# Kernel tuning notes

Hardware: AMD Instinct MI355X
Metric: run time of the kernel (lower is better)

The kernel has to match this reference:

```python
import math
import jax, jax.numpy as jnp
import numpy as np

VOCAB = 80; MAX_SEQ_LEN = 32; D_MODEL = 512; NHEAD = 8; DFF = 2048; NLAYERS = 6
EOS = 1; SOS = 2; PAD = 0; BATCH = 8; MEM_LEN = 256; PE_LEN = MAX_SEQ_LEN + 2
EPS = 1e-5


def _sinusoid(max_len, d):
    pos = np.arange(max_len)[:, None].astype(np.float32)
    div = np.exp(np.arange(0, d, 2).astype(np.float32) * -(math.log(10000.0) / d))
    pe = np.zeros((max_len, d), np.float32)
    pe[:, 0::2] = np.sin(pos * div)
    pe[:, 1::2] = np.cos(pos * div)
    return jnp.asarray(pe)


def setup_inputs() -> dict:
    key = jax.random.key(0)
    ks = jax.random.split(key, 10)
    s = 0.02
    def n(k, shape, scale=s):
        return jax.random.normal(k, shape, jnp.float32) * scale
    return {
        "memory": n(ks[0], (BATCH, MEM_LEN, D_MODEL), 1.0),
        "emb_table": n(ks[1], (VOCAB, D_MODEL), 1.0),
        "pe": _sinusoid(PE_LEN, D_MODEL),
        "sa_in_w": n(ks[2], (NLAYERS, 3 * D_MODEL, D_MODEL)),
        "sa_in_b": jnp.zeros((NLAYERS, 3 * D_MODEL), jnp.float32),
        "sa_out_w": n(ks[3], (NLAYERS, D_MODEL, D_MODEL)),
        "sa_out_b": jnp.zeros((NLAYERS, D_MODEL), jnp.float32),
        "ca_in_w": n(ks[4], (NLAYERS, 3 * D_MODEL, D_MODEL)),
        "ca_in_b": jnp.zeros((NLAYERS, 3 * D_MODEL), jnp.float32),
        "ca_out_w": n(ks[5], (NLAYERS, D_MODEL, D_MODEL)),
        "ca_out_b": jnp.zeros((NLAYERS, D_MODEL), jnp.float32),
        "ln_w": jnp.ones((NLAYERS, 3, D_MODEL), jnp.float32),
        "ln_b": jnp.zeros((NLAYERS, 3, D_MODEL), jnp.float32),
        "ff1_w": n(ks[6], (NLAYERS, DFF, D_MODEL)),
        "ff1_b": jnp.zeros((NLAYERS, DFF), jnp.float32),
        "ff2_w": n(ks[7], (NLAYERS, D_MODEL, DFF)),
        "ff2_b": jnp.zeros((NLAYERS, D_MODEL), jnp.float32),
        "clf_w": n(ks[8], (VOCAB, D_MODEL)),
        "clf_b": jnp.zeros((VOCAB,), jnp.float32),
    }


def _layer_norm(x, g, b):
    mu = jnp.mean(x, -1, keepdims=True)
    var = jnp.mean((x - mu) ** 2, -1, keepdims=True)
    return (x - mu) * jax.lax.rsqrt(var + EPS) * g + b


def _mha(q_in, kv_in, in_w, in_b, out_w, out_b, mask):
    d = q_in.shape[-1]; hd = d // NHEAD
    wq, wk, wv = jnp.split(in_w, 3, 0)
    bq, bk, bv = jnp.split(in_b, 3)
    B, Tq, _ = q_in.shape; Tk = kv_in.shape[1]
    q = (q_in @ wq.T + bq).reshape(B, Tq, NHEAD, hd)
    k = (kv_in @ wk.T + bk).reshape(B, Tk, NHEAD, hd)
    v = (kv_in @ wv.T + bv).reshape(B, Tk, NHEAD, hd)
    scores = jnp.einsum('bqhd,bkhd->bhqk', q, k) / math.sqrt(hd)
    if mask is not None:
        scores = jnp.where(mask, -1e9, scores)
    probs = jax.nn.softmax(scores, -1)
    out = jnp.einsum('bhqk,bkhd->bqhd', probs, v).reshape(B, Tq, d)
    return out @ out_w.T + out_b


def _decoder(tgt, memory, causal, p):
    # post-norm TransformerDecoder (torch default, dropout=identity at inference)
    x = tgt
    for l in range(NLAYERS):
        x = _layer_norm(x + _mha(x, x, p['sa_in_w'][l], p['sa_in_b'][l], p['sa_out_w'][l], p['sa_out_b'][l], causal), p['ln_w'][l, 0], p['ln_b'][l, 0])
        x = _layer_norm(x + _mha(x, memory, p['ca_in_w'][l], p['ca_in_b'][l], p['ca_out_w'][l], p['ca_out_b'][l], None), p['ln_w'][l, 1], p['ln_b'][l, 1])
        h = jax.nn.gelu(x @ p['ff1_w'][l].T + p['ff1_b'][l], approximate=False)
        x = _layer_norm(x + h @ p['ff2_w'][l].T + p['ff2_b'][l], p['ln_w'][l, 2], p['ln_b'][l, 2])
    return x


def _greedy(memory, emb_table, pe, p, clf_w, clf_b):
    B = memory.shape[0]; T1 = MAX_SEQ_LEN + 1
    sq = math.sqrt(D_MODEL)
    causal = jnp.triu(jnp.ones((T1, T1), bool), 1)[None, None]  # True = blocked
    tgt0 = jnp.zeros((B, T1, D_MODEL), memory.dtype)
    tgt0 = tgt0.at[:, 0].set(pe[0] + emb_table[SOS] * sq)

    def step(tgt, t):
        # full recompute of the whole decoder stack each step (no KV cache),
        # causal mask makes position t depend only on the valid prefix.
        out = _decoder(tgt, memory, causal, p)
        out_t = jax.lax.dynamic_slice_in_dim(out, t, 1, 1)[:, 0]
        logits = out_t @ clf_w.T + clf_b
        pred = jnp.argmax(logits, -1)
        # original uses pe[len(sampled_ids)] == pe[t+2] for the token at slot t+1
        new_e = jnp.take(pe, t + 2, axis=0) + emb_table[pred] * sq
        tgt = jax.lax.dynamic_update_slice_in_dim(tgt, new_e[:, None, :], t + 1, 1)
        return tgt, (logits, pred)

    _, (logits, preds) = jax.lax.scan(step, tgt0, jnp.arange(MAX_SEQ_LEN))
    all_logits = jnp.transpose(logits, (1, 0, 2))  # [B, T, V]
    sampled = jnp.concatenate([jnp.full((B, 1), SOS, preds.dtype), preds.T], 1)
    eos_idx = jnp.argmax(sampled == EOS, 1)  # first eos (0 if none, as torch)
    sampled = jnp.where(jnp.arange(T1)[None] <= eos_idx[:, None], PAD, sampled)
    return all_logits, sampled


def reference(memory, emb_table, pe, sa_in_w, sa_in_b, sa_out_w, sa_out_b, ca_in_w, ca_in_b, ca_out_w, ca_out_b, ln_w, ln_b, ff1_w, ff1_b, ff2_w, ff2_b, clf_w, clf_b):
    p = dict(sa_in_w=sa_in_w, sa_in_b=sa_in_b, sa_out_w=sa_out_w, sa_out_b=sa_out_b,
             ca_in_w=ca_in_w, ca_in_b=ca_in_b, ca_out_w=ca_out_w, ca_out_b=ca_out_b,
             ln_w=ln_w, ln_b=ln_b, ff1_w=ff1_w, ff1_b=ff1_b, ff2_w=ff2_w, ff2_b=ff2_b)
    return _greedy(memory, emb_table, pe, p, clf_w, clf_b)
```

## Files before the change

kernel.cpp:

```cpp
#include <hip/hip_runtime.h>
#include <math.h>

constexpr int T1 = 33, NL = 6, VOC = 80;
constexpr float SQD = 22.62741699796952f;

__device__ float g_memk[(size_t)NL * 2048 * 512];
__device__ float g_memv[(size_t)NL * 2048 * 512];
__device__ float g_kc[(size_t)NL * 8 * T1 * 512];
__device__ float g_vc[(size_t)NL * 8 * T1 * 512];
__device__ float g_x[8 * 512], g_x2[8 * 512], g_y[8 * 512], g_q[8 * 512], g_att[8 * 512];
__device__ float g_h[8 * 2048];
__device__ int   g_tok[8 * T1];

struct DecP {
  const float *mem, *emb, *pe, *saw, *sab, *sow, *sob, *caw, *cab, *cow, *cob,
              *lnw, *lnb, *f1w, *f1b, *f2w, *f2b, *cw, *cb;
  float* out;
};

__global__ __launch_bounds__(256) void k_memkv(const float* __restrict__ mem,
                                               const float* __restrict__ caw,
                                               const float* __restrict__ cab) {
  __shared__ float mlds[128][34];
  __shared__ float wlds[256][34];
  const int tid = threadIdx.x;
  const int l = blockIdx.x / 64, rem = blockIdx.x % 64;
  const int mt = rem >> 2, rt = rem & 3;
  const float* wbase = caw + (size_t)l * 1536 * 512 + (size_t)512 * 512;

  float acc[8][16];
#pragma unroll
  for (int i = 0; i < 8; ++i)
#pragma unroll
    for (int j = 0; j < 16; ++j) acc[i][j] = 0.f;

  const int tm = tid >> 4, tr = tid & 15;

  for (int kb = 0; kb < 16; ++kb) {
    __syncthreads();
    {
      int row = tid >> 1, half = tid & 1;
      const float2* src = (const float2*)(mem + (size_t)(mt * 128 + row) * 512 + kb * 32 + half * 16);
      float2* dst = (float2*)&mlds[row][half * 16];
#pragma unroll
      for (int q = 0; q < 8; ++q) dst[q] = src[q];
    }
    {
      int c2 = (tid & 15) * 2, rb = tid >> 4;
#pragma unroll
      for (int q = 0; q < 16; ++q) {
        int row = rb + 16 * q;
        *(float2*)&wlds[row][c2] =
            *(const float2*)(wbase + (size_t)(rt * 256 + row) * 512 + kb * 32 + c2);
      }
    }
    __syncthreads();
#pragma unroll 4
    for (int k2 = 0; k2 < 16; ++k2) {
      float2 mv[8];
#pragma unroll
      for (int i = 0; i < 8; ++i) mv[i] = *(const float2*)&mlds[tm * 8 + i][2 * k2];
#pragma unroll
      for (int j = 0; j < 16; ++j) {
        float2 w2 = *(const float2*)&wlds[tr + 16 * j][2 * k2];
#pragma unroll
        for (int i = 0; i < 8; ++i) acc[i][j] += mv[i].x * w2.x + mv[i].y * w2.y;
      }
    }
  }
#pragma unroll
  for (int i = 0; i < 8; ++i) {
    int mrow = mt * 128 + tm * 8 + i;
#pragma unroll
    for (int j = 0; j < 16; ++j) {
      int r = rt * 256 + tr + 16 * j;
      float v = acc[i][j] + cab[l * 1536 + 512 + r];
      if (r < 512) g_memk[((size_t)l * 2048 + mrow) * 512 + r] = v;
      else         g_memv[((size_t)l * 2048 + mrow) * 512 + (r - 512)] = v;
    }
  }
}

__device__ __forceinline__ float wave_reduce8(const float (&acc)[8], int lane) {
  float a0, a1, a2, a3;
  {
    bool hi = lane & 1;
    float s0 = hi ? acc[0] : acc[1], s1 = hi ? acc[2] : acc[3];
    float s2 = hi ? acc[4] : acc[5], s3 = hi ? acc[6] : acc[7];
    float r0 = __shfl_xor(s0, 1), r1 = __shfl_xor(s1, 1);
    float r2 = __shfl_xor(s2, 1), r3 = __shfl_xor(s3, 1);
    a0 = (hi ? acc[1] : acc[0]) + r0;  a1 = (hi ? acc[3] : acc[2]) + r1;
    a2 = (hi ? acc[5] : acc[4]) + r2;  a3 = (hi ? acc[7] : acc[6]) + r3;
  }
  float b0, b1;
  {
    bool hi = lane & 2;
    float s0 = hi ? a0 : a1, s1 = hi ? a2 : a3;
    float r0 = __shfl_xor(s0, 2), r1 = __shfl_xor(s1, 2);
    b0 = (hi ? a1 : a0) + r0;  b1 = (hi ? a3 : a2) + r1;
  }
  float f;
  {
    bool hi = lane & 4;
    float s = hi ? b0 : b1;
    float r = __shfl_xor(s, 4);
    f = (hi ? b1 : b0) + r;
  }
  f += __shfl_xor(f, 8);  f += __shfl_xor(f, 16);  f += __shfl_xor(f, 32);
  return f;
}

__device__ __forceinline__ void stage_in(float (*sx)[520], const float* __restrict__ g,
                                         bool doLN, const float* __restrict__ lw,
                                         const float* __restrict__ lb, float* __restrict__ wb) {
  const int tid = threadIdx.x;
#pragma unroll
  for (int q = 0; q < 4; ++q) {
    int f4 = tid + 256 * q;
    int b = f4 >> 7, c = (f4 & 127) << 2;
    float4 v = ((const float4*)g)[f4];
    *(float4*)&sx[b][c] = v;
  }
  __syncthreads();
  if (doLN) {
    const int lane = tid & 63, wv = tid >> 6;
#pragma unroll
    for (int rr = 0; rr < 2; ++rr) {
      int b = wv + 4 * rr;
      float vals[8]; float sm = 0.f;
#pragma unroll
      for (int j = 0; j < 8; ++j) { vals[j] = sx[b][lane + 64 * j]; sm += vals[j]; }
#pragma unroll
      for (int o = 32; o; o >>= 1) sm += __shfl_xor(sm, o);
      float mu = sm * (1.f / 512.f);
      float s2 = 0.f;
#pragma unroll
      for (int j = 0; j < 8; ++j) { float d = vals[j] - mu; s2 += d * d; }
#pragma unroll
      for (int o = 32; o; o >>= 1) s2 += __shfl_xor(s2, o);
      float rstd = 1.f / sqrtf(s2 * (1.f / 512.f) + 1e-5f);
#pragma unroll
      for (int j = 0; j < 8; ++j) {
        int c = lane + 64 * j;
        sx[b][c] = (vals[j] - mu) * rstd * lw[c] + lb[c];
      }
    }
    __syncthreads();
  }
  if (wb && blockIdx.x == 0) {
#pragma unroll
    for (int q = 0; q < 4; ++q) {
      int f4 = tid + 256 * q;
      int b = f4 >> 7, c = (f4 & 127) << 2;
      ((float4*)wb)[f4] = *(float4*)&sx[b][c];
    }
  }
}

template <int MODE>
__device__ __forceinline__ void gemv512(float (*sx)[520], const float* __restrict__ W,
                                        const float* __restrict__ bias, int rpb,
                                        float* __restrict__ out, const float* __restrict__ res,
                                        int l, int t) {
  const int lane = threadIdx.x & 63, wv = threadIdx.x >> 6;
  const int r0 = blockIdx.x * rpb;
  for (int rr = wv; rr < rpb; rr += 4) {
    const int r = r0 + rr;
    const float* wr = W + (size_t)r * 512;
    float acc[8] = {0, 0, 0, 0, 0, 0, 0, 0};
#pragma unroll
    for (int j = 0; j < 8; ++j) {
      float w = wr[lane + 64 * j];
#pragma unroll
      for (int b = 0; b < 8; ++b) acc[b] += w * sx[b][lane + 64 * j];
    }
    float f = wave_reduce8(acc, lane);
    if (lane < 8) {
      const int b = lane;
      float v = f + bias[r];
      if constexpr (MODE == 0) {
        if (r < 512)       out[b * 512 + r] = v;
        else if (r < 1024) g_kc[(((size_t)l * 8 + b) * T1 + t) * 512 + (r - 512)] = v;
        else               g_vc[(((size_t)l * 8 + b) * T1 + t) * 512 + (r - 1024)] = v;
      } else if constexpr (MODE == 1) {
        out[b * 512 + r] = v + res[b * 512 + r];
      } else if constexpr (MODE == 2) {
        out[b * 512 + r] = v;
      } else {
        out[b * 2048 + r] = 0.5f * v * (1.f + erff(v * 0.70710678118654752f));
      }
    }
  }
}

__device__ __forceinline__ void stage_h(float (*sb)[2052]) {
  const int tid = threadIdx.x;
#pragma unroll
  for (int q = 0; q < 16; ++q) {
    int f4 = tid + 256 * q;
    int b = f4 >> 9, c = (f4 & 511) << 2;
    *(float4*)&sb[b][c] = ((const float4*)g_h)[f4];
  }
}

__device__ __forceinline__ void gemvH(float (*sb)[2052], const float* __restrict__ W,
                                      const float* __restrict__ bias,
                                      const float* __restrict__ res, float* __restrict__ out) {
  const int lane = threadIdx.x & 63, wv = threadIdx.x >> 6;
  const int r0 = blockIdx.x * 8;
  for (int rr = wv; rr < 8; rr += 4) {
    const int r = r0 + rr;
    const float* wr = W + (size_t)r * 2048;
    float acc[8] = {0, 0, 0, 0, 0, 0, 0, 0};
#pragma unroll 8
    for (int j = 0; j < 32; ++j) {
      float w = wr[lane + 64 * j];
#pragma unroll
      for (int b = 0; b < 8; ++b) acc[b] += w * sb[b][lane + 64 * j];
    }
    float f = wave_reduce8(acc, lane);
    if (lane < 8) out[lane * 512 + r] = f + bias[r] + res[lane * 512 + r];
  }
}

__global__ __launch_bounds__(256) void k_start(DecP P) {
  int b = blockIdx.x;
#pragma unroll
  for (int q = 0; q < 2; ++q) {
    int c = threadIdx.x + 256 * q;
    g_x[b * 512 + c] = P.pe[c] + P.emb[2 * 512 + c] * SQD;
  }
  if (threadIdx.x == 0) g_tok[b * T1] = 2;
}

__global__ __launch_bounds__(256) void k_A(DecP P, int l, int t) {
  __shared__ float sx[8][520];
  const float* lw = (l > 0) ? P.lnw + ((l - 1) * 3 + 2) * 512 : P.lnw;
  const float* lb = (l > 0) ? P.lnb + ((l - 1) * 3 + 2) * 512 : P.lnb;
  stage_in(sx, (l == 0) ? g_x : g_y, l > 0, lw, lb, (l > 0) ? g_x : nullptr);
  gemv512<0>(sx, P.saw + (size_t)l * 1536 * 512, P.sab + l * 1536, 8, g_q, nullptr, l, t);
}

__global__ __launch_bounds__(64) void k_B(DecP P, int l, int t) {
  __shared__ float s_p[128];
  const int lane = threadIdx.x;
  const int b = blockIdx.x >> 3, h = blockIdx.x & 7;
  s_p[lane] = g_q[b * 512 + h * 64 + lane];
  asm volatile("s_waitcnt lgkmcnt(0)" ::: "memory");
  __builtin_amdgcn_sched_barrier(0);
  float sc = -3.4e38f;
  if (lane <= t) {
    const float4* kr = (const float4*)&g_kc[(((size_t)l * 8 + b) * T1 + lane) * 512 + h * 64];
    float s = 0.f;
#pragma unroll
    for (int d4 = 0; d4 < 16; ++d4) {
      float4 kv = kr[d4];
      s += s_p[d4 * 4 + 0] * kv.x + s_p[d4 * 4 + 1] * kv.y +
           s_p[d4 * 4 + 2] * kv.z + s_p[d4 * 4 + 3] * kv.w;
    }
    sc = s * 0.125f;
  }
  float m = sc;
#pragma unroll
  for (int o = 32; o; o >>= 1) m = fmaxf(m, __shfl_xor(m, o));
  float ex = (lane <= t) ? expf(sc - m) : 0.f;
  float sum = ex;
#pragma unroll
  for (int o = 32; o; o >>= 1) sum += __shfl_xor(sum, o);
  s_p[64 + lane] = ex / sum;
  asm volatile("s_waitcnt lgkmcnt(0)" ::: "memory");
  __builtin_amdgcn_sched_barrier(0);
  float o = 0.f;
  for (int j = 0; j <= t; ++j)
    o += s_p[64 + j] * g_vc[(((size_t)l * 8 + b) * T1 + j) * 512 + h * 64 + lane];
  g_att[b * 512 + h * 64 + lane] = o;
}

__global__ __launch_bounds__(256) void k_C(DecP P, int l) {
  __shared__ float sx[8][520];
  stage_in(sx, g_att, false, nullptr, nullptr, nullptr);
  gemv512<1>(sx, P.sow + (size_t)l * 512 * 512, P.sob + l * 512, 8, g_y, g_x, l, 0);
}

__global__ __launch_bounds__(256) void k_D(DecP P, int l) {
  __shared__ float sx[8][520];
  stage_in(sx, g_y, true, P.lnw + (l * 3 + 0) * 512, P.lnb + (l * 3 + 0) * 512, g_x2);
  gemv512<2>(sx, P.caw + (size_t)l * 1536 * 512, P.cab + l * 1536, 8, g_q, nullptr, l, 0);
}

__global__ __launch_bounds__(256) void k_E(DecP P, int l) {
  __shared__ float s_p[336];
  __shared__ float s_w[4][2];
  __shared__ float s_pv[4][64];
  const int tid = threadIdx.x;
  const int lane = tid & 63, wv = tid >> 6;
  const int b = blockIdx.x >> 3, h = blockIdx.x & 7;
  if (tid < 64) s_p[tid] = g_q[b * 512 + h * 64 + tid];
  __syncthreads();
  int m0 = wv * 64 + lane;
  const float4* kr = (const float4*)&g_memk[((size_t)l * 2048 + b * 256 + m0) * 512 + h * 64];
  float s = 0.f;
#pragma unroll
  for (int d4 = 0; d4 < 16; ++d4) {
    float4 kv = kr[d4];
    s += s_p[d4 * 4 + 0] * kv.x + s_p[d4 * 4 + 1] * kv.y +
         s_p[d4 * 4 + 2] * kv.z + s_p[d4 * 4 + 3] * kv.w;
  }
  s *= 0.125f;
  float m = s;
#pragma unroll
  for (int o = 32; o; o >>= 1) m = fmaxf(m, __shfl_xor(m, o));
  if (lane == 0) s_w[wv][0] = m;
  __syncthreads();
  float M = fmaxf(fmaxf(s_w[0][0], s_w[1][0]), fmaxf(s_w[2][0], s_w[3][0]));
  float ex = expf(s - M);
  float sum = ex;
#pragma unroll
  for (int o = 32; o; o >>= 1) sum += __shfl_xor(sum, o);
  if (lane == 0) s_w[wv][1] = sum;
  __syncthreads();
  float S = s_w[0][1] + s_w[1][1] + s_w[2][1] + s_w[3][1];
  s_p[64 + m0] = ex / S;
  __syncthreads();
  float o = 0.f;
  const float* vbase = &g_memv[((size_t)l * 2048 + b * 256) * 512 + h * 64];
  for (int j = 0; j < 64; ++j) {
    int mm = wv * 64 + j;
    o += s_p[64 + mm] * vbase[(size_t)mm * 512 + lane];
  }
  s_pv[wv][lane] = o;
  __syncthreads();
  if (wv == 0) {
    float tot = s_pv[0][lane] + s_pv[1][lane] + s_pv[2][lane] + s_pv[3][lane];
    g_att[b * 512 + h * 64 + lane] = tot;
  }
}

__global__ __launch_bounds__(256) void k_F(DecP P, int l) {
  __shared__ float sx[8][520];
  stage_in(sx, g_att, false, nullptr, nullptr, nullptr);
  gemv512<1>(sx, P.cow + (size_t)l * 512 * 512, P.cob + l * 512, 8, g_y, g_x2, l, 0);
}

__global__ __launch_bounds__(256) void k_G(DecP P, int l) {
  __shared__ float sx[8][520];
  stage_in(sx, g_y, true, P.lnw + (l * 3 + 1) * 512, P.lnb + (l * 3 + 1) * 512, g_x2);
  gemv512<3>(sx, P.f1w + (size_t)l * 2048 * 512, P.f1b + l * 2048, 8, g_h, nullptr, l, 0);
}

__global__ __launch_bounds__(256) void k_H(DecP P, int l) {
  __shared__ float sb[8][2052];
  stage_h(sb);
  __syncthreads();
  gemvH(sb, P.f2w + (size_t)l * 512 * 2048, P.f2b + l * 512, g_x2, g_y);
}

__global__ __launch_bounds__(256) void k_T(DecP P, int t) {
  __shared__ float sx[8][520];
  __shared__ float s_p[80];
  __shared__ int s_int[1];
  const int tid = threadIdx.x;
  const int lane = tid & 63, wv = tid >> 6;
  const int b = blockIdx.x;
  stage_in(sx, g_y, true, P.lnw + (5 * 3 + 2) * 512, P.lnb + (5 * 3 + 2) * 512, nullptr);
  for (int i = 0; i < 20; ++i) {
    int r = wv * 20 + i;
    const float* wr = P.cw + (size_t)r * 512;
    float a = 0.f;
#pragma unroll
    for (int j = 0; j < 8; ++j) a += wr[lane + 64 * j] * sx[b][lane + 64 * j];
#pragma unroll
    for (int o = 32; o; o >>= 1) a += __shfl_xor(a, o);
    if (lane == 0) {
      float v = a + P.cb[r];
      s_p[r] = v;
      P.out[((size_t)b * 32 + t) * VOC + r] = v;
    }
  }
  __syncthreads();
  if (wv == 0) {
    float v1 = s_p[lane];
    int i1 = lane;
    if (lane < 16) {
      float v2 = s_p[64 + lane];
      if (v2 > v1) { v1 = v2; i1 = 64 + lane; }
    }
#pragma unroll
    for (int o = 32; o; o >>= 1) {
      float ov = __shfl_xor(v1, o);
      int oi = __shfl_xor(i1, o);
      if (ov > v1 || (ov == v1 && oi < i1)) { v1 = ov; i1 = oi; }
    }
    if (lane == 0) { s_int[0] = i1; g_tok[b * T1 + t + 1] = i1; }
  }
  __syncthreads();
  int pred = s_int[0];
#pragma unroll
  for (int q = 0; q < 2; ++q) {
    int c = tid + 256 * q;
    g_x[b * 512 + c] = P.pe[(t + 2) * 512 + c] + P.emb[(size_t)pred * 512 + c] * SQD;
  }
}

__global__ __launch_bounds__(64) void k_out(DecP P) {
  int lane = threadIdx.x;
  if (lane < 8) {
    int b = lane;
    int eos = -1;
    for (int j = 0; j < T1; ++j) {
      int tk = g_tok[b * T1 + j];
      if (tk == 1 && eos < 0) eos = j;
    }
    if (eos < 0) eos = 0;
    for (int j = 0; j < T1; ++j) {
      int tk = g_tok[b * T1 + j];
      P.out[20480 + b * T1 + j] = (j <= eos) ? 0.f : (float)tk;
    }
  }
}

extern "C" void kernel_launch(void* const* d_in, const int* in_sizes, int n_in,
                              void* d_out, int out_size, void* d_ws, size_t ws_size,
                              hipStream_t stream) {
  (void)in_sizes; (void)n_in; (void)d_ws; (void)ws_size; (void)out_size;
  const float* mem = (const float*)d_in[0];
  const float* emb = (const float*)d_in[1];
  const float* pe  = (const float*)d_in[2];
  const float* saw = (const float*)d_in[3];
  const float* sab = (const float*)d_in[4];
  const float* sow = (const float*)d_in[5];
  const float* sob = (const float*)d_in[6];
  const float* caw = (const float*)d_in[7];
  const float* cab = (const float*)d_in[8];
  const float* cow = (const float*)d_in[9];
  const float* cob = (const float*)d_in[10];
  const float* lnw = (const float*)d_in[11];
  const float* lnb = (const float*)d_in[12];
  const float* f1w = (const float*)d_in[13];
  const float* f1b = (const float*)d_in[14];
  const float* f2w = (const float*)d_in[15];
  const float* f2b = (const float*)d_in[16];
  const float* cw  = (const float*)d_in[17];
  const float* cb  = (const float*)d_in[18];

  DecP P{mem, emb, pe, saw, sab, sow, sob, caw, cab, cow, cob,
         lnw, lnb, f1w, f1b, f2w, f2b, cw, cb, (float*)d_out};

  hipLaunchKernelGGL(k_start, dim3(8), dim3(256), 0, stream, P);
  hipLaunchKernelGGL(k_memkv, dim3(384), dim3(256), 0, stream, mem, caw, cab);

  for (int t = 0; t < 32; ++t) {
    for (int l = 0; l < NL; ++l) {
      hipLaunchKernelGGL(k_A, dim3(192), dim3(256), 0, stream, P, l, t);
      hipLaunchKernelGGL(k_B, dim3(64), dim3(64), 0, stream, P, l, t);
      hipLaunchKernelGGL(k_C, dim3(64), dim3(256), 0, stream, P, l);
      hipLaunchKernelGGL(k_D, dim3(64), dim3(256), 0, stream, P, l);
      hipLaunchKernelGGL(k_E, dim3(64), dim3(256), 0, stream, P, l);
      hipLaunchKernelGGL(k_F, dim3(64), dim3(256), 0, stream, P, l);
      hipLaunchKernelGGL(k_G, dim3(256), dim3(256), 0, stream, P, l);
      hipLaunchKernelGGL(k_H, dim3(64), dim3(256), 0, stream, P, l);
    }
    hipLaunchKernelGGL(k_T, dim3(8), dim3(256), 0, stream, P, t);
  }
  hipLaunchKernelGGL(k_out, dim3(1), dim3(64), 0, stream, P);
}
```

Measured before the change: 8.999 ms.

## Fuse decoder layer into three per-(batch,head) kernels with double-precision partial sums

Replaces the eight launches per layer with three fused kernels, each run by 64 blocks with one block per (batch, head). Each kernel does the projection, attention and output projection for its head and writes per-head partial sums. The next kernel reduces those partials and fuses bias, residual and LayerNorm. Memory K/V is relaid as [l][b][h][m][d] so each head's slice is contiguous. All accumulation moves to double precision, presumably so greedy argmax tokens match the reference, but FP64 math and the extra partial-sum traffic add cost that may offset the launch savings.

After: 34.63 ms. +284.9%, slower.

```diff
diff --git a/kernel.cpp b/kernel.cpp
--- a/kernel.cpp
+++ b/kernel.cpp
@@ -4,12 +4,16 @@
 constexpr int T1 = 33, NL = 6, VOC = 80;
 constexpr float SQD = 22.62741699796952f;
 
-__device__ float g_memk[(size_t)NL * 2048 * 512];
-__device__ float g_memv[(size_t)NL * 2048 * 512];
+__device__ float g_memk[(size_t)NL * 8 * 8 * 256 * 64];
+__device__ float g_memv[(size_t)NL * 8 * 8 * 256 * 64];
 __device__ float g_kc[(size_t)NL * 8 * T1 * 512];
 __device__ float g_vc[(size_t)NL * 8 * T1 * 512];
-__device__ float g_x[8 * 512], g_x2[8 * 512], g_y[8 * 512], g_q[8 * 512], g_att[8 * 512];
-__device__ float g_h[8 * 2048];
+__device__ float g_cur[8 * 512];
+__device__ float g_x2[8 * 512];
+__device__ float g_x3[8 * 512];
+__device__ double g_part1[8 * 512 * 8];
+__device__ double g_part2[8 * 512 * 8];
+__device__ double g_part3[8 * 512 * 8];
 __device__ int   g_tok[8 * T1];
 
 struct DecP {
@@ -71,156 +75,82 @@
 #pragma unroll
   for (int i = 0; i < 8; ++i) {
     int mrow = mt * 128 + tm * 8 + i;
+    int bb = mrow >> 8, mm = mrow & 255;
 #pragma unroll
     for (int j = 0; j < 16; ++j) {
       int r = rt * 256 + tr + 16 * j;
       float v = acc[i][j] + cab[l * 1536 + 512 + r];
-      if (r < 512) g_memk[((size_t)l * 2048 + mrow) * 512 + r] = v;
-      else         g_memv[((size_t)l * 2048 + mrow) * 512 + (r - 512)] = v;
-    }
-  }
-}
-
-__device__ __forceinline__ float wave_reduce8(const float (&acc)[8], int lane) {
-  float a0, a1, a2, a3;
+      if (r < 512) {
+        int hh = r >> 6, d = r & 63;
+        g_memk[((((size_t)l * 8 + bb) * 8 + hh) * 256 + mm) * 64 + d] = v;
+      } else {
+        int r2 = r - 512, hh = r2 >> 6, d = r2 & 63;
+        g_memv[((((size_t)l * 8 + bb) * 8 + hh) * 256 + mm) * 64 + d] = v;
+      }
+    }
+  }
+}
+
+__device__ __forceinline__ double wave_reduce8d(const double (&acc)[8], int lane) {
+  double a0, a1, a2, a3;
   {
     bool hi = lane & 1;
-    float s0 = hi ? acc[0] : acc[1], s1 = hi ? acc[2] : acc[3];
-    float s2 = hi ? acc[4] : acc[5], s3 = hi ? acc[6] : acc[7];
-    float r0 = __shfl_xor(s0, 1), r1 = __shfl_xor(s1, 1);
-    float r2 = __shfl_xor(s2, 1), r3 = __shfl_xor(s3, 1);
+    double s0 = hi ? acc[0] : acc[1], s1 = hi ? acc[2] : acc[3];
+    double s2 = hi ? acc[4] : acc[5], s3 = hi ? acc[6] : acc[7];
+    double r0 = __shfl_xor(s0, 1), r1 = __shfl_xor(s1, 1);
+    double r2 = __shfl_xor(s2, 1), r3 = __shfl_xor(s3, 1);
     a0 = (hi ? acc[1] : acc[0]) + r0;  a1 = (hi ? acc[3] : acc[2]) + r1;
     a2 = (hi ? acc[5] : acc[4]) + r2;  a3 = (hi ? acc[7] : acc[6]) + r3;
   }
-  float b0, b1;
+  double b0, b1;
   {
     bool hi = lane & 2;
-    float s0 = hi ? a0 : a1, s1 = hi ? a2 : a3;
-    float r0 = __shfl_xor(s0, 2), r1 = __shfl_xor(s1, 2);
+    double s0 = hi ? a0 : a1, s1 = hi ? a2 : a3;
+    double r0 = __shfl_xor(s0, 2), r1 = __shfl_xor(s1, 2);
     b0 = (hi ? a1 : a0) + r0;  b1 = (hi ? a3 : a2) + r1;
   }
-  float f;
+  double f;
   {
     bool hi = lane & 4;
-    float s = hi ? b0 : b1;
-    float r = __shfl_xor(s, 4);
+    double s = hi ? b0 : b1;
+    double r = __shfl_xor(s, 4);
     f = (hi ? b1 : b0) + r;
   }
   f += __shfl_xor(f, 8);  f += __shfl_xor(f, 16);  f += __shfl_xor(f, 32);
   return f;
 }
 
-__device__ __forceinline__ void stage_in(float (*sx)[520], const float* __restrict__ g,
-                                         bool doLN, const float* __restrict__ lw,
-                                         const float* __restrict__ lb, float* __restrict__ wb) {
-  const int tid = threadIdx.x;
-#pragma unroll
-  for (int q = 0; q < 4; ++q) {
-    int f4 = tid + 256 * q;
-    int b = f4 >> 7, c = (f4 & 127) << 2;
-    float4 v = ((const float4*)g)[f4];
-    *(float4*)&sx[b][c] = v;
-  }
-  __syncthreads();
-  if (doLN) {
-    const int lane = tid & 63, wv = tid >> 6;
-#pragma unroll
-    for (int rr = 0; rr < 2; ++rr) {
-      int b = wv + 4 * rr;
-      float vals[8]; float sm = 0.f;
-#pragma unroll
-      for (int j = 0; j < 8; ++j) { vals[j] = sx[b][lane + 64 * j]; sm += vals[j]; }
-#pragma unroll
-      for (int o = 32; o; o >>= 1) sm += __shfl_xor(sm, o);
-      float mu = sm * (1.f / 512.f);
-      float s2 = 0.f;
-#pragma unroll
-      for (int j = 0; j < 8; ++j) { float d = vals[j] - mu; s2 += d * d; }
-#pragma unroll
-      for (int o = 32; o; o >>= 1) s2 += __shfl_xor(s2, o);
-      float rstd = 1.f / sqrtf(s2 * (1.f / 512.f) + 1e-5f);
-#pragma unroll
-      for (int j = 0; j < 8; ++j) {
-        int c = lane + 64 * j;
-        sx[b][c] = (vals[j] - mu) * rstd * lw[c] + lb[c];
-      }
-    }
-    __syncthreads();
-  }
-  if (wb && blockIdx.x == 0) {
-#pragma unroll
-    for (int q = 0; q < 4; ++q) {
-      int f4 = tid + 256 * q;
-      int b = f4 >> 7, c = (f4 & 127) << 2;
-      ((float4*)wb)[f4] = *(float4*)&sx[b][c];
-    }
-  }
-}
-
-template <int MODE>
-__device__ __forceinline__ void gemv512(float (*sx)[520], const float* __restrict__ W,
-                                        const float* __restrict__ bias, int rpb,
-                                        float* __restrict__ out, const float* __restrict__ res,
-                                        int l, int t) {
-  const int lane = threadIdx.x & 63, wv = threadIdx.x >> 6;
-  const int r0 = blockIdx.x * rpb;
-  for (int rr = wv; rr < rpb; rr += 4) {
-    const int r = r0 + rr;
-    const float* wr = W + (size_t)r * 512;
-    float acc[8] = {0, 0, 0, 0, 0, 0, 0, 0};
-#pragma unroll
-    for (int j = 0; j < 8; ++j) {
-      float w = wr[lane + 64 * j];
-#pragma unroll
-      for (int b = 0; b < 8; ++b) acc[b] += w * sx[b][lane + 64 * j];
-    }
-    float f = wave_reduce8(acc, lane);
-    if (lane < 8) {
-      const int b = lane;
-      float v = f + bias[r];
-      if constexpr (MODE == 0) {
-        if (r < 512)       out[b * 512 + r] = v;
-        else if (r < 1024) g_kc[(((size_t)l * 8 + b) * T1 + t) * 512 + (r - 512)] = v;
-        else               g_vc[(((size_t)l * 8 + b) * T1 + t) * 512 + (r - 1024)] = v;
-      } else if constexpr (MODE == 1) {
-        out[b * 512 + r] = v + res[b * 512 + r];
-      } else if constexpr (MODE == 2) {
-        out[b * 512 + r] = v;
-      } else {
-        out[b * 2048 + r] = 0.5f * v * (1.f + erff(v * 0.70710678118654752f));
-      }
-    }
-  }
-}
-
-__device__ __forceinline__ void stage_h(float (*sb)[2052]) {
-  const int tid = threadIdx.x;
-#pragma unroll
-  for (int q = 0; q < 16; ++q) {
-    int f4 = tid + 256 * q;
-    int b = f4 >> 9, c = (f4 & 511) << 2;
-    *(float4*)&sb[b][c] = ((const float4*)g_h)[f4];
-  }
-}
-
-__device__ __forceinline__ void gemvH(float (*sb)[2052], const float* __restrict__ W,
-                                      const float* __restrict__ bias,
-                                      const float* __restrict__ res, float* __restrict__ out) {
-  const int lane = threadIdx.x & 63, wv = threadIdx.x >> 6;
-  const int r0 = blockIdx.x * 8;
-  for (int rr = wv; rr < 8; rr += 4) {
-    const int r = r0 + rr;
-    const float* wr = W + (size_t)r * 2048;
-    float acc[8] = {0, 0, 0, 0, 0, 0, 0, 0};
-#pragma unroll 8
-    for (int j = 0; j < 32; ++j) {
-      float w = wr[lane + 64 * j];
-#pragma unroll
-      for (int b = 0; b < 8; ++b) acc[b] += w * sb[b][lane + 64 * j];
-    }
-    float f = wave_reduce8(acc, lane);
-    if (lane < 8) out[lane * 512 + r] = f + bias[r] + res[lane * 512 + r];
-  }
+__device__ __forceinline__ void reduce_ln_dev(const double* __restrict__ part,
+                                              const float* __restrict__ bias,
+                                              const float* __restrict__ resg,
+                                              const float* __restrict__ lw,
+                                              const float* __restrict__ lb,
+                                              float* s_x, double* s_redd,
+                                              int b, bool wr, float* __restrict__ wg) {
+  const int tid = threadIdx.x, lane = tid & 63, wv = tid >> 6;
+  const double* p0 = part + ((size_t)(b * 512 + tid) << 3);
+  const double* p1 = part + ((size_t)(b * 512 + tid + 256) << 3);
+  double s0 = 0.0, s1 = 0.0;
+#pragma unroll
+  for (int hh = 0; hh < 8; ++hh) { s0 += p0[hh]; s1 += p1[hh]; }
+  float v0 = (float)(s0 + (double)bias[tid]) + resg[b * 512 + tid];
+  float v1 = (float)(s1 + (double)bias[tid + 256]) + resg[b * 512 + tid + 256];
+  double sm = (double)v0 + (double)v1;
+  double sq = (double)v0 * (double)v0 + (double)v1 * (double)v1;
+#pragma unroll
+  for (int o = 32; o; o >>= 1) { sm += __shfl_xor(sm, o); sq += __shfl_xor(sq, o); }
+  if (lane == 0) { s_redd[wv] = sm; s_redd[4 + wv] = sq; }
+  __syncthreads();
+  double S = (s_redd[0] + s_redd[1]) + (s_redd[2] + s_redd[3]);
+  double Q = (s_redd[4] + s_redd[5]) + (s_redd[6] + s_redd[7]);
+  double mu = S * (1.0 / 512.0);
+  double var = Q * (1.0 / 512.0) - mu * mu;
+  double rstd = 1.0 / sqrt(var + 1e-5);
+  float f0 = (float)(((double)v0 - mu) * rstd * (double)lw[tid] + (double)lb[tid]);
+  float f1 = (float)(((double)v1 - mu) * rstd * (double)lw[tid + 256] + (double)lb[tid + 256]);
+  s_x[tid] = f0; s_x[tid + 256] = f1;
+  if (wr) { wg[b * 512 + tid] = f0; wg[b * 512 + tid + 256] = f1; }
+  __syncthreads();
 }
 
 __global__ __launch_bounds__(256) void k_start(DecP P) {
@@ -228,156 +158,277 @@
 #pragma unroll
   for (int q = 0; q < 2; ++q) {
     int c = threadIdx.x + 256 * q;
-    g_x[b * 512 + c] = P.pe[c] + P.emb[2 * 512 + c] * SQD;
+    g_cur[b * 512 + c] = P.pe[c] + P.emb[2 * 512 + c] * SQD;
   }
   if (threadIdx.x == 0) g_tok[b * T1] = 2;
 }
 
-__global__ __launch_bounds__(256) void k_A(DecP P, int l, int t) {
-  __shared__ float sx[8][520];
-  const float* lw = (l > 0) ? P.lnw + ((l - 1) * 3 + 2) * 512 : P.lnw;
-  const float* lb = (l > 0) ? P.lnb + ((l - 1) * 3 + 2) * 512 : P.lnb;
-  stage_in(sx, (l == 0) ? g_x : g_y, l > 0, lw, lb, (l > 0) ? g_x : nullptr);
-  gemv512<0>(sx, P.saw + (size_t)l * 1536 * 512, P.sab + l * 1536, 8, g_q, nullptr, l, t);
-}
-
-__global__ __launch_bounds__(64) void k_B(DecP P, int l, int t) {
+__global__ __launch_bounds__(256) void kP1(DecP P, int l, int t) {
+  __shared__ float s_x[512];
+  __shared__ float s_q[64];
+  __shared__ float s_att[64];
   __shared__ float s_p[128];
-  const int lane = threadIdx.x;
-  const int b = blockIdx.x >> 3, h = blockIdx.x & 7;
-  s_p[lane] = g_q[b * 512 + h * 64 + lane];
-  asm volatile("s_waitcnt lgkmcnt(0)" ::: "memory");
-  __builtin_amdgcn_sched_barrier(0);
-  float sc = -3.4e38f;
-  if (lane <= t) {
-    const float4* kr = (const float4*)&g_kc[(((size_t)l * 8 + b) * T1 + lane) * 512 + h * 64];
-    float s = 0.f;
-#pragma unroll
-    for (int d4 = 0; d4 < 16; ++d4) {
-      float4 kv = kr[d4];
-      s += s_p[d4 * 4 + 0] * kv.x + s_p[d4 * 4 + 1] * kv.y +
-           s_p[d4 * 4 + 2] * kv.z + s_p[d4 * 4 + 3] * kv.w;
-    }
-    sc = s * 0.125f;
-  }
-  float m = sc;
-#pragma unroll
-  for (int o = 32; o; o >>= 1) m = fmaxf(m, __shfl_xor(m, o));
-  float ex = (lane <= t) ? expf(sc - m) : 0.f;
-  float sum = ex;
-#pragma unroll
-  for (int o = 32; o; o >>= 1) sum += __shfl_xor(sum, o);
-  s_p[64 + lane] = ex / sum;
-  asm volatile("s_waitcnt lgkmcnt(0)" ::: "memory");
-  __builtin_amdgcn_sched_barrier(0);
-  float o = 0.f;
-  for (int j = 0; j <= t; ++j)
-    o += s_p[64 + j] * g_vc[(((size_t)l * 8 + b) * T1 + j) * 512 + h * 64 + lane];
-  g_att[b * 512 + h * 64 + lane] = o;
-}
-
-__global__ __launch_bounds__(256) void k_C(DecP P, int l) {
-  __shared__ float sx[8][520];
-  stage_in(sx, g_att, false, nullptr, nullptr, nullptr);
-  gemv512<1>(sx, P.sow + (size_t)l * 512 * 512, P.sob + l * 512, 8, g_y, g_x, l, 0);
-}
-
-__global__ __launch_bounds__(256) void k_D(DecP P, int l) {
-  __shared__ float sx[8][520];
-  stage_in(sx, g_y, true, P.lnw + (l * 3 + 0) * 512, P.lnb + (l * 3 + 0) * 512, g_x2);
-  gemv512<2>(sx, P.caw + (size_t)l * 1536 * 512, P.cab + l * 1536, 8, g_q, nullptr, l, 0);
-}
-
-__global__ __launch_bounds__(256) void k_E(DecP P, int l) {
-  __shared__ float s_p[336];
-  __shared__ float s_w[4][2];
-  __shared__ float s_pv[4][64];
+  __shared__ double s_redd[8];
   const int tid = threadIdx.x;
   const int lane = tid & 63, wv = tid >> 6;
   const int b = blockIdx.x >> 3, h = blockIdx.x & 7;
-  if (tid < 64) s_p[tid] = g_q[b * 512 + h * 64 + tid];
-  __syncthreads();
-  int m0 = wv * 64 + lane;
-  const float4* kr = (const float4*)&g_memk[((size_t)l * 2048 + b * 256 + m0) * 512 + h * 64];
-  float s = 0.f;
-#pragma unroll
-  for (int d4 = 0; d4 < 16; ++d4) {
-    float4 kv = kr[d4];
-    s += s_p[d4 * 4 + 0] * kv.x + s_p[d4 * 4 + 1] * kv.y +
-         s_p[d4 * 4 + 2] * kv.z + s_p[d4 * 4 + 3] * kv.w;
-  }
-  s *= 0.125f;
-  float m = s;
-#pragma unroll
-  for (int o = 32; o; o >>= 1) m = fmaxf(m, __shfl_xor(m, o));
-  if (lane == 0) s_w[wv][0] = m;
-  __syncthreads();
-  float M = fmaxf(fmaxf(s_w[0][0], s_w[1][0]), fmaxf(s_w[2][0], s_w[3][0]));
-  float ex = expf(s - M);
-  float sum = ex;
-#pragma unroll
-  for (int o = 32; o; o >>= 1) sum += __shfl_xor(sum, o);
-  if (lane == 0) s_w[wv][1] = sum;
-  __syncthreads();
-  float S = s_w[0][1] + s_w[1][1] + s_w[2][1] + s_w[3][1];
-  s_p[64 + m0] = ex / S;
-  __syncthreads();
-  float o = 0.f;
-  const float* vbase = &g_memv[((size_t)l * 2048 + b * 256) * 512 + h * 64];
-  for (int j = 0; j < 64; ++j) {
-    int mm = wv * 64 + j;
-    o += s_p[64 + mm] * vbase[(size_t)mm * 512 + lane];
-  }
-  s_pv[wv][lane] = o;
-  __syncthreads();
+
+  if (l == 0) {
+    float2 v = ((const float2*)(g_cur + b * 512))[tid];
+    s_x[2 * tid] = v.x; s_x[2 * tid + 1] = v.y;
+    __syncthreads();
+  } else {
+    reduce_ln_dev(g_part3, P.f2b + (l - 1) * 512, g_x3,
+                  P.lnw + ((l - 1) * 3 + 2) * 512, P.lnb + ((l - 1) * 3 + 2) * 512,
+                  s_x, s_redd, b, h == 0, g_cur);
+  }
+
+  {
+    const float* Wl = P.saw + (size_t)l * 1536 * 512;
+    const float* Bl = P.sab + l * 1536;
+#pragma unroll 2
+    for (int it = 0; it < 6; ++it) {
+      int u0 = it * 32 + wv * 8;
+      double acc[8];
+#pragma unroll
+      for (int i = 0; i < 8; ++i) {
+        int u = u0 + i, sec = u >> 6, dd = u & 63;
+        const float* wr = Wl + (size_t)(sec * 512 + h * 64 + dd) * 512;
+        double a = 0.0;
+#pragma unroll
+        for (int j = 0; j < 8; ++j) a += (double)wr[lane + 64 * j] * (double)s_x[lane + 64 * j];
+        acc[i] = a;
+      }
+      double f = wave_reduce8d(acc, lane);
+      if (lane < 8) {
+        int u = u0 + lane, sec = u >> 6, dd = u & 63;
+        float v = (float)(f + (double)Bl[sec * 512 + h * 64 + dd]);
+        if (sec == 0) s_q[dd] = v;
+        else if (sec == 1) g_kc[(((size_t)l * 8 + b) * T1 + t) * 512 + h * 64 + dd] = v;
+        else               g_vc[(((size_t)l * 8 + b) * T1 + t) * 512 + h * 64 + dd] = v;
+      }
+    }
+  }
+  __syncthreads();
+
   if (wv == 0) {
-    float tot = s_pv[0][lane] + s_pv[1][lane] + s_pv[2][lane] + s_pv[3][lane];
-    g_att[b * 512 + h * 64 + lane] = tot;
-  }
-}
-
-__global__ __launch_bounds__(256) void k_F(DecP P, int l) {
-  __shared__ float sx[8][520];
-  stage_in(sx, g_att, false, nullptr, nullptr, nullptr);
-  gemv512<1>(sx, P.cow + (size_t)l * 512 * 512, P.cob + l * 512, 8, g_y, g_x2, l, 0);
-}
-
-__global__ __launch_bounds__(256) void k_G(DecP P, int l) {
-  __shared__ float sx[8][520];
-  stage_in(sx, g_y, true, P.lnw + (l * 3 + 1) * 512, P.lnb + (l * 3 + 1) * 512, g_x2);
-  gemv512<3>(sx, P.f1w + (size_t)l * 2048 * 512, P.f1b + l * 2048, 8, g_h, nullptr, l, 0);
-}
-
-__global__ __launch_bounds__(256) void k_H(DecP P, int l) {
-  __shared__ float sb[8][2052];
-  stage_h(sb);
-  __syncthreads();
-  gemvH(sb, P.f2w + (size_t)l * 512 * 2048, P.f2b + l * 512, g_x2, g_y);
-}
-
-__global__ __launch_bounds__(256) void k_T(DecP P, int t) {
-  __shared__ float sx[8][520];
+    float sc = -3.4e38f;
+    if (lane <= t) {
+      const float* kr = &g_kc[(((size_t)l * 8 + b) * T1 + lane) * 512 + h * 64];
+      double s = 0.0;
+#pragma unroll
+      for (int j = 0; j < 64; ++j) s += (double)s_q[j] * (double)kr[j];
+      sc = (float)(s * 0.125);
+    }
+    float m = sc;
+#pragma unroll
+    for (int o = 32; o; o >>= 1) m = fmaxf(m, __shfl_xor(m, o));
+    double ex = (lane <= t) ? exp((double)sc - (double)m) : 0.0;
+    double sum = ex;
+#pragma unroll
+    for (int o = 32; o; o >>= 1) sum += __shfl_xor(sum, o);
+    s_p[lane] = (float)(ex / sum);
+    asm volatile("s_waitcnt lgkmcnt(0)" ::: "memory");
+    __builtin_amdgcn_sched_barrier(0);
+    const float* vb = &g_vc[(((size_t)l * 8 + b) * T1) * 512 + h * 64 + lane];
+    double o1 = 0.0;
+    for (int j = 0; j <= t; ++j) o1 += (double)s_p[j] * (double)vb[(size_t)j * 512];
+    s_att[lane] = (float)o1;
+  }
+  __syncthreads();
+
+  {
+    const float* Wo = P.sow + (size_t)l * 512 * 512 + h * 64;
+    double r_att = (double)s_att[lane];
+#pragma unroll 2
+    for (int it = 0; it < 16; ++it) {
+      int d0 = it * 32 + wv * 8;
+      double acc[8];
+#pragma unroll
+      for (int i = 0; i < 8; ++i) acc[i] = (double)Wo[(size_t)(d0 + i) * 512 + lane] * r_att;
+      double f = wave_reduce8d(acc, lane);
+      if (lane < 8) g_part1[((size_t)(b * 512 + d0 + lane) << 3) + h] = f;
+    }
+  }
+}
+
+__global__ __launch_bounds__(256) void kP2(DecP P, int l) {
+  __shared__ float s_x[512];
+  __shared__ float s_q[64];
+  __shared__ float s_att[64];
+  __shared__ float s_prob[256];
+  __shared__ double s_redd[8];
+  __shared__ double s_pvd[4][64];
+  __shared__ float s_mx[4];
+  const int tid = threadIdx.x;
+  const int lane = tid & 63, wv = tid >> 6;
+  const int b = blockIdx.x >> 3, h = blockIdx.x & 7;
+
+  reduce_ln_dev(g_part1, P.sob + l * 512, g_cur,
+                P.lnw + (l * 3 + 0) * 512, P.lnb + (l * 3 + 0) * 512,
+                s_x, s_redd, b, h == 0, g_x2);
+
+  {
+    const float* Wq = P.caw + (size_t)l * 1536 * 512 + (size_t)(h * 64) * 512;
+    const float* Bq = P.cab + l * 1536 + h * 64;
+#pragma unroll
+    for (int it = 0; it < 2; ++it) {
+      int d0 = it * 32 + wv * 8;
+      double acc[8];
+#pragma unroll
+      for (int i = 0; i < 8; ++i) {
+        const float* wr = Wq + (size_t)(d0 + i) * 512;
+        double a = 0.0;
+#pragma unroll
+        for (int j = 0; j < 8; ++j) a += (double)wr[lane + 64 * j] * (double)s_x[lane + 64 * j];
+        acc[i] = a;
+      }
+      double f = wave_reduce8d(acc, lane);
+      if (lane < 8) s_q[d0 + lane] = (float)(f + (double)Bq[d0 + lane]);
+    }
+  }
+  __syncthreads();
+
+  {
+    size_t slice = (((size_t)l * 8 + b) * 8 + h) * 256;
+    int p = wv * 64 + lane;
+    const float4* kr = (const float4*)(g_memk + (slice + p) * 64);
+    double s = 0.0;
+#pragma unroll
+    for (int j = 0; j < 16; ++j) {
+      float4 kv = kr[j];
+      s += (double)s_q[4 * j] * (double)kv.x + (double)s_q[4 * j + 1] * (double)kv.y +
+           (double)s_q[4 * j + 2] * (double)kv.z + (double)s_q[4 * j + 3] * (double)kv.w;
+    }
+    float sc = (float)(s * 0.125);
+    float m = sc;
+#pragma unroll
+    for (int o = 32; o; o >>= 1) m = fmaxf(m, __shfl_xor(m, o));
+    if (lane == 0) s_mx[wv] = m;
+    __syncthreads();
+    float M = fmaxf(fmaxf(s_mx[0], s_mx[1]), fmaxf(s_mx[2], s_mx[3]));
+    double ex = exp((double)sc - (double)M);
+    double sum = ex;
+#pragma unroll
+    for (int o = 32; o; o >>= 1) sum += __shfl_xor(sum, o);
+    if (lane == 0) s_redd[4 + wv] = sum;
+    __syncthreads();
+    double S = (s_redd[4] + s_redd[5]) + (s_redd[6] + s_redd[7]);
+    s_prob[p] = (float)(ex / S);
+    __syncthreads();
+    double acc = 0.0;
+    const float* vb = g_memv + (slice + wv * 64) * 64 + lane;
+#pragma unroll 8
+    for (int j = 0; j < 64; ++j) acc += (double)s_prob[wv * 64 + j] * (double)vb[(size_t)j * 64];
+    s_pvd[wv][lane] = acc;
+    __syncthreads();
+    if (wv == 0)
+      s_att[lane] = (float)((s_pvd[0][lane] + s_pvd[1][lane]) + (s_pvd[2][lane] + s_pvd[3][lane]));
+  }
+  __syncthreads();
+
+  {
+    const float* Wo = P.cow + (size_t)l * 512 * 512 + h * 64;
+    double r_att = (double)s_att[lane];
+#pragma unroll 2
+    for (int it = 0; it < 16; ++it) {
+      int d0 = it * 32 + wv * 8;
+      double acc[8];
+#pragma unroll
+      for (int i = 0; i < 8; ++i) acc[i] = (double)Wo[(size_t)(d0 + i) * 512 + lane] * r_att;
+      double f = wave_reduce8d(acc, lane);
+      if (lane < 8) g_part2[((size_t)(b * 512 + d0 + lane) << 3) + h] = f;
+    }
+  }
+}
+
+__global__ __launch_bounds__(256) void kP3(DecP P, int l) {
+  __shared__ float s_x[512];
+  __shared__ float s_h1[256];
+  __shared__ double s_redd[8];
+  const int tid = threadIdx.x;
+  const int lane = tid & 63, wv = tid >> 6;
+  const int b = blockIdx.x >> 3, h = blockIdx.x & 7;
+
+  reduce_ln_dev(g_part2, P.cob + l * 512, g_x2,
+                P.lnw + (l * 3 + 1) * 512, P.lnb + (l * 3 + 1) * 512,
+                s_x, s_redd, b, h == 0, g_x3);
+
+  {
+    const float* W1 = P.f1w + (size_t)l * 2048 * 512 + (size_t)(h * 256) * 512;
+    const float* B1 = P.f1b + l * 2048 + h * 256;
+#pragma unroll 2
+    for (int it = 0; it < 8; ++it) {
+      int d0 = it * 32 + wv * 8;
+      double acc[8];
+#pragma unroll
+      for (int i = 0; i < 8; ++i) {
+        const float* wr = W1 + (size_t)(d0 + i) * 512;
+        double a = 0.0;
+#pragma unroll
+        for (int j = 0; j < 8; ++j) a += (double)wr[lane + 64 * j] * (double)s_x[lane + 64 * j];
+        acc[i] = a;
+      }
+      double f = wave_reduce8d(acc, lane);
+      if (lane < 8) {
+        int dl = d0 + lane;
+        float pre = (float)(f + (double)B1[dl]);
+        double pv = (double)pre;
+        s_h1[dl] = (float)(0.5 * pv * (1.0 + erf(pv * 0.7071067811865475244)));
+      }
+    }
+  }
+  __syncthreads();
+
+  {
+    const float* W2 = P.f2w + (size_t)l * 512 * 2048 + h * 256;
+#pragma unroll 2
+    for (int it = 0; it < 16; ++it) {
+      int d0 = it * 32 + wv * 8;
+      double acc[8];
+#pragma unroll
+      for (int i = 0; i < 8; ++i) {
+        const float* wr = W2 + (size_t)(d0 + i) * 2048;
+        double a = 0.0;
+#pragma unroll
+        for (int j = 0; j < 4; ++j) a += (double)wr[lane + 64 * j] * (double)s_h1[lane + 64 * j];
+        acc[i] = a;
+      }
+      double f = wave_reduce8d(acc, lane);
+      if (lane < 8) g_part3[((size_t)(b * 512 + d0 + lane) << 3) + h] = f;
+    }
+  }
+}
+
+__global__ __launch_bounds__(256) void kT(DecP P, int t) {
+  __shared__ float s_x[512];
   __shared__ float s_p[80];
+  __shared__ double s_redd[8];
   __shared__ int s_int[1];
   const int tid = threadIdx.x;
   const int lane = tid & 63, wv = tid >> 6;
   const int b = blockIdx.x;
-  stage_in(sx, g_y, true, P.lnw + (5 * 3 + 2) * 512, P.lnb + (5 * 3 + 2) * 512, nullptr);
+
+  reduce_ln_dev(g_part3, P.f2b + 5 * 512, g_x3,
+                P.lnw + 17 * 512, P.lnb + 17 * 512,
+                s_x, s_redd, b, false, nullptr);
+
   for (int i = 0; i < 20; ++i) {
     int r = wv * 20 + i;
     const float* wr = P.cw + (size_t)r * 512;
-    float a = 0.f;
-#pragma unroll
-    for (int j = 0; j < 8; ++j) a += wr[lane + 64 * j] * sx[b][lane + 64 * j];
+    double a = 0.0;
+#pragma unroll
+    for (int j = 0; j < 8; ++j) a += (double)wr[lane + 64 * j] * (double)s_x[lane + 64 * j];
 #pragma unroll
     for (int o = 32; o; o >>= 1) a += __shfl_xor(a, o);
     if (lane == 0) {
-      float v = a + P.cb[r];
+      float v = (float)(a + (double)P.cb[r]);
       s_p[r] = v;
       P.out[((size_t)b * 32 + t) * VOC + r] = v;
     }
   }
   __syncthreads();
+
   if (wv == 0) {
     float v1 = s_p[lane];
     int i1 = lane;
@@ -398,7 +449,7 @@
 #pragma unroll
   for (int q = 0; q < 2; ++q) {
     int c = tid + 256 * q;
-    g_x[b * 512 + c] = P.pe[(t + 2) * 512 + c] + P.emb[(size_t)pred * 512 + c] * SQD;
+    g_cur[b * 512 + c] = P.pe[(t + 2) * 512 + c] + P.emb[(size_t)pred * 512 + c] * SQD;
   }
 }
 
@@ -451,16 +502,11 @@
 
   for (int t = 0; t < 32; ++t) {
     for (int l = 0; l < NL; ++l) {
-      hipLaunchKernelGGL(k_A, dim3(192), dim3(256), 0, stream, P, l, t);
-      hipLaunchKernelGGL(k_B, dim3(64), dim3(64), 0, stream, P, l, t);
-      hipLaunchKernelGGL(k_C, dim3(64), dim3(256), 0, stream, P, l);
-      hipLaunchKernelGGL(k_D, dim3(64), dim3(256), 0, stream, P, l);
-      hipLaunchKernelGGL(k_E, dim3(64), dim3(256), 0, stream, P, l);
-      hipLaunchKernelGGL(k_F, dim3(64), dim3(256), 0, stream, P, l);
-      hipLaunchKernelGGL(k_G, dim3(256), dim3(256), 0, stream, P, l);
-      hipLaunchKernelGGL(k_H, dim3(64), dim3(256), 0, stream, P, l);
-    }
-    hipLaunchKernelGGL(k_T, dim3(8), dim3(256), 0, stream, P, t);
+      hipLaunchKernelGGL(kP1, dim3(64), dim3(256), 0, stream, P, l, t);
+      hipLaunchKernelGGL(kP2, dim3(64), dim3(256), 0, stream, P, l);
+      hipLaunchKernelGGL(kP3, dim3(64), dim3(256), 0, stream, P, l);
+    }
+    hipLaunchKernelGGL(kT, dim3(8), dim3(256), 0, stream, P, t);
   }
   hipLaunchKernelGGL(k_out, dim3(1), dim3(64), 0, stream, P);
 }
```
